# Kernel tuning notes

Hardware: AMD Instinct MI355X
Metric: run time of the kernel (lower is better)

Reference implementation:

```python
import jax, jax.numpy as jnp
import numpy as np


def setup_inputs() -> dict:
    key = jax.random.key(0)
    ks = jax.random.split(key, 7)
    B, N, Fin, Fout = 32, 1024, 64, 64
    s = 1.0 / np.sqrt(Fin)
    return {
        "X": jax.random.normal(ks[0], (B, N, Fin), dtype=jnp.float32),
        "A": jax.random.normal(ks[1], (B, N, N), dtype=jnp.float32),  # unused in forward, kept for signature fidelity
        "W": jax.random.uniform(ks[2], (Fin, Fout), jnp.float32, -s, s),
        "att_W": jax.random.uniform(ks[3], (Fin, Fout), jnp.float32, -s, s),
        "a": jax.random.uniform(ks[4], (Fout, Fout), jnp.float32, -s, s),
        "bias_W": jax.random.uniform(ks[5], (Fout,), jnp.float32, -s, s),
        "self_W": jax.random.uniform(ks[6], (Fin, Fout), jnp.float32, -s, s),
    }


def reference(X, A, W, att_W, a, bias_W, self_W):
    # att_X = X @ att_W : [B, N, Fout]
    att_X = jnp.einsum('bnf,fg->bng', X, att_W)
    # torch einsum 'ij,ajk->ajk' sums `a` over i => per-feature scale a.sum(0)
    scale = jnp.sum(a, axis=0)  # [Fout]
    # Z[b,i,k] = sum_j att_X[b,i,j] * scale[j] * att_X[b,k,j]  -> [B, N, N]
    Z = jnp.einsum('big,bkg->bik', att_X * scale, att_X)
    n = Z.shape[1]
    Z = Z * (1.0 - jnp.eye(n, dtype=Z.dtype))  # zero diagonal per batch
    att = jax.nn.leaky_relu(Z, negative_slope=0.01)
    # H = att @ (X W) + bias_W + X self_W
    XW = jnp.einsum('bnf,fg->bng', X, W)
    H = jnp.einsum('bnm,bmg->bng', att, XW) + bias_W
    H = H + jnp.einsum('bnf,fg->bng', X, self_W)
    return H
```

## Files before the change

### kernel.cpp

```cpp
#include <hip/hip_runtime.h>

#define DEV __device__ __forceinline__
typedef short s16x8 __attribute__((ext_vector_type(8)));
typedef float f32x16 __attribute__((ext_vector_type(16)));
typedef unsigned short u16;

#define WAIT_VMCNT(N) asm volatile("s_waitcnt vmcnt(" #N ")" ::: "memory")
#define CFENCE asm volatile("" ::: "memory")

DEV unsigned cvt_pk_bf16(float lo, float hi) {
  unsigned r;
  asm volatile("v_cvt_pk_bf16_f32 %0, %1, %2" : "=v"(r) : "v"(lo), "v"(hi));
  return r;
}
DEV u16 f2bf(float f) {
  unsigned u = __builtin_bit_cast(unsigned, f);
  unsigned r = u + 0x7fffu + ((u >> 16) & 1u);
  return (u16)(r >> 16);
}
DEV float bf2f(u16 u) { return __builtin_bit_cast(float, (unsigned)u << 16); }
DEV f32x16 zero16() {
  f32x16 v;
  #pragma unroll
  for (int i = 0; i < 16; ++i) v[i] = 0.f;
  return v;
}

DEV void gld16(const u16* g, u16* l) {
  __builtin_amdgcn_global_load_lds(
      (const __attribute__((address_space(1))) void*)g,
      (__attribute__((address_space(3))) void*)l, 16, 0, 0);
}

DEV void stage_tile64(const u16* __restrict__ gbase, size_t stride, u16* lbuf, int t) {
  #pragma unroll
  for (int p = 0; p < 2; ++p) {
    int c = p * 256 + t;
    int row = c >> 3, s = c & 7;
    int gck = s ^ (row & 7);
    const u16* src = gbase + (size_t)row * stride + gck * 8;
    u16* dst = lbuf + (size_t)(p * 256 + (t & 192)) * 8;
    gld16(src, dst);
  }
}

DEV s16x8 frag(const u16* buf, int row, int chunk) {
  return *(const s16x8*)(buf + row * 64 + ((chunk ^ (row & 7)) << 3));
}

DEV int kswz(int row, int d) {
  return row * 64 + ((((d >> 3) ^ (row & 7)) << 3) | (d & 7));
}

__global__ __launch_bounds__(256) void wprep_kernel(
    const float* __restrict__ attW, const float* __restrict__ W,
    const float* __restrict__ selfW, const float* __restrict__ Aa,
    u16* __restrict__ Wsw, float* __restrict__ scal_ws) {
  __shared__ __align__(16) u16 T[64 * 72];
  __shared__ float sc4[4][64];
  const int t = threadIdx.x, bi = blockIdx.x;

  if (bi == 0) {
    int qt = t >> 6, d = t & 63;
    float s = 0.f;
    #pragma unroll
    for (int i = 0; i < 16; ++i) s += Aa[(qt * 16 + i) * 64 + d];
    sc4[qt][d] = s;
  }

  const float* src = (bi == 0) ? attW : (bi == 1) ? W : selfW;
  #pragma unroll
  for (int p = 0; p < 4; ++p) {
    int c = p * 256 + t;
    int f = c >> 4, g0 = (c & 15) * 4;
    float4 v = *(const float4*)(src + f * 64 + g0);
    T[(g0 + 0) * 72 + f] = f2bf(v.x);
    T[(g0 + 1) * 72 + f] = f2bf(v.y);
    T[(g0 + 2) * 72 + f] = f2bf(v.z);
    T[(g0 + 3) * 72 + f] = f2bf(v.w);
  }
  __syncthreads();
  #pragma unroll
  for (int p = 0; p < 2; ++p) {
    int c = p * 256 + t;
    int g = c >> 3, f0 = (c & 7) * 8;
    *(s16x8*)&Wsw[bi * 4096 + g * 64 + f0] = *(const s16x8*)&T[g * 72 + f0];
  }
  if (bi == 0 && t < 64)
    scal_ws[t] = sc4[0][t] + sc4[1][t] + sc4[2][t] + sc4[3][t];
}

__global__ __launch_bounds__(256) void prep_kernel(
    const float* __restrict__ X, const u16* __restrict__ Wsw,
    const float* __restrict__ scal_ws, const float* __restrict__ biasW,
    u16* __restrict__ Kbf, u16* __restrict__ Qbf, u16* __restrict__ Vt,
    u16* __restrict__ Bb) {
  __shared__ __align__(16) u16 Xl[64 * 64];
  __shared__ __align__(16) u16 WtL[3][64 * 64];
  __shared__ __align__(16) u16 Ql[64 * 64];
  __shared__ __align__(16) u16 Bl[64 * 64];
  __shared__ __align__(16) u16 Vl[64 * 72];

  const int t = threadIdx.x;
  const int r0 = blockIdx.x * 64;
  const int b = r0 >> 10;
  const int n0 = r0 & 1023;
  const int lane = t & 63, w = t >> 6, h = lane >> 5, ln = lane & 31;
  const int rg = (w >> 1) * 32;
  const int cf = w & 1;
  const int d = cf * 32 + ln;

  #pragma unroll
  for (int i = 0; i < 3; ++i) stage_tile64(Wsw + i * 4096, 64, &WtL[i][0], t);

  const float sc_d = scal_ws[d];
  const float bi = biasW[d];

  #pragma unroll
  for (int p = 0; p < 2; ++p) {
    int c = p * 256 + t;
    int row = c >> 3, ck = c & 7;
    const float4* src = (const float4*)(X + (size_t)(r0 + row) * 64 + ck * 8);
    float4 a0 = src[0], a1 = src[1];
    unsigned* dst = (unsigned*)&Xl[row * 64 + ((ck ^ (row & 7)) << 3)];
    dst[0] = cvt_pk_bf16(a0.x, a0.y);
    dst[1] = cvt_pk_bf16(a0.z, a0.w);
    dst[2] = cvt_pk_bf16(a1.x, a1.y);
    dst[3] = cvt_pk_bf16(a1.z, a1.w);
  }
  __syncthreads();

  s16x8 xa[4];
  #pragma unroll
  for (int ks = 0; ks < 4; ++ks) xa[ks] = frag(Xl, rg + ln, ks * 2 + h);

  f32x16 aA = zero16(), aW = zero16(), aS = zero16();
  #pragma unroll
  for (int ks = 0; ks < 4; ++ks) {
    s16x8 bA = frag(&WtL[0][0], d, ks * 2 + h);
    s16x8 bW = frag(&WtL[1][0], d, ks * 2 + h);
    s16x8 bS = frag(&WtL[2][0], d, ks * 2 + h);
    aA = __builtin_amdgcn_mfma_f32_32x32x16_bf16(xa[ks], bA, aA, 0, 0, 0);
    aW = __builtin_amdgcn_mfma_f32_32x32x16_bf16(xa[ks], bW, aW, 0, 0, 0);
    aS = __builtin_amdgcn_mfma_f32_32x32x16_bf16(xa[ks], bS, aS, 0, 0, 0);
  }
  __syncthreads();

  #pragma unroll
  for (int reg = 0; reg < 16; ++reg) {
    int rl = (reg & 3) + 8 * (reg >> 2) + 4 * h;
    int row = rg + rl;
    Xl[kswz(row, d)] = f2bf(aA[reg]);
    Ql[kswz(row, d)] = f2bf(aA[reg] * sc_d);
    Bl[kswz(row, d)] = f2bf(aS[reg] + bi);
  }
  #pragma unroll
  for (int pg = 0; pg < 4; ++pg) {
    int n = rg + pg * 8 + 4 * h;
    *(unsigned*)&Vl[d * 72 + n] = cvt_pk_bf16(aW[pg * 4 + 0], aW[pg * 4 + 1]);
    *(unsigned*)&Vl[d * 72 + n + 2] = cvt_pk_bf16(aW[pg * 4 + 2], aW[pg * 4 + 3]);
  }
  __syncthreads();

  #pragma unroll
  for (int p = 0; p < 2; ++p) {
    int c = p * 256 + t;
    int row = c >> 3, ck = c & 7;
    size_t go = (size_t)(r0 + row) * 64 + ck * 8;
    int lo = row * 64 + ((ck ^ (row & 7)) << 3);
    *(s16x8*)&Kbf[go] = *(const s16x8*)&Xl[lo];
    *(s16x8*)&Qbf[go] = *(const s16x8*)&Ql[lo];
    *(s16x8*)&Bb[go] = *(const s16x8*)&Bl[lo];
  }
  #pragma unroll
  for (int p = 0; p < 2; ++p) {
    int c = p * 256 + t;
    int dd = c >> 3, ck = c & 7;
    *(s16x8*)&Vt[(size_t)(b * 64 + dd) * 1024 + n0 + ck * 8] =
        *(const s16x8*)&Vl[dd * 72 + ck * 8];
  }
}

#define PROC(SV, DG, PWV)                                                      \
  do {                                                                         \
    float p_[16];                                                              \
    _Pragma("unroll") for (int r_ = 0; r_ < 16; ++r_) {                        \
      float v_ = (SV)[r_];                                                     \
      p_[r_] = fmaxf(v_, 0.f) + 0.01f * fminf(v_, 0.f);                        \
    }                                                                          \
    if (DG) {                                                                  \
      _Pragma("unroll") for (int r_ = 0; r_ < 16; ++r_) {                      \
        int rl_ = (r_ & 3) + 8 * (r_ >> 2) + 4 * h;                            \
        p_[r_] = (rl_ == ln) ? 0.f : p_[r_];                                   \
      }                                                                        \
    }                                                                          \
    unsigned pk_[8];                                                           \
    _Pragma("unroll") for (int i_ = 0; i_ < 8; ++i_)                           \
        pk_[i_] = cvt_pk_bf16(p_[2 * i_], p_[2 * i_ + 1]);                     \
    auto a0_ = __builtin_amdgcn_permlane32_swap(pk_[0], pk_[2], false, false); \
    auto a1_ = __builtin_amdgcn_permlane32_swap(pk_[1], pk_[3], false, false); \
    auto a2_ = __builtin_amdgcn_permlane32_swap(pk_[4], pk_[6], false, false); \
    auto a3_ = __builtin_amdgcn_permlane32_swap(pk_[5], pk_[7], false, false); \
    PWV[0][0] = a0_[0]; PWV[0][1] = a1_[0]; PWV[0][2] = a0_[1];                \
    PWV[0][3] = a1_[1]; PWV[1][0] = a2_[0]; PWV[1][1] = a3_[0];                \
    PWV[1][2] = a2_[1]; PWV[1][3] = a3_[1];                                    \
  } while (0)

__global__ __launch_bounds__(256) void attn_kernel(
    const u16* __restrict__ Qbf, const u16* __restrict__ Kbf,
    const u16* __restrict__ Vt, const u16* __restrict__ Bb,
    float* __restrict__ Hout) {
  __shared__ __align__(16) u16 KV[3][2][64 * 64];
  float* Ol0 = (float*)&KV[0][0][0];
  float* Ol1 = (float*)&KV[1][0][0];

  const int t = threadIdx.x;
  const int b = blockIdx.x;
  const int q0 = blockIdx.y * 64;
  const int lane = t & 63, w = t >> 6, h = lane >> 5, ln = lane & 31;
  const int qh = w & 1, kvh = w >> 1;
  const int qg = q0 + qh * 32 + ln;

  const u16* Qg = Qbf + (size_t)b * 65536;
  const u16* Kg = Kbf + (size_t)b * 65536;
  const u16* Vg = Vt + (size_t)b * 65536;

  s16x8 qf[4];
  #pragma unroll
  for (int ks = 0; ks < 4; ++ks)
    qf[ks] = *(const s16x8*)(Qg + (size_t)qg * 64 + ks * 16 + h * 8);

  stage_tile64(Kg, 64, &KV[0][0][0], t);
  stage_tile64(Vg, 1024, &KV[0][1][0], t);
  stage_tile64(Kg + (size_t)64 * 64, 64, &KV[1][0][0], t);
  stage_tile64(Vg + 64, 1024, &KV[1][1][0], t);

  f32x16 o0 = zero16(), o1 = zero16();

  #pragma unroll 1
  for (int tix = 0; tix < 16; ++tix) {
    const int kv0 = tix * 64;
    if (tix < 15) {
      WAIT_VMCNT(4);
    } else {
      WAIT_VMCNT(0);
    }
    __builtin_amdgcn_s_barrier();
    CFENCE;
    if (tix < 14) {
      const int ns = (tix + 2) % 3;
      stage_tile64(Kg + (size_t)(kv0 + 128) * 64, 64, &KV[ns][0][0], t);
      stage_tile64(Vg + (kv0 + 128), 1024, &KV[ns][1][0], t);
    }
    const u16* Kl = &KV[tix % 3][0][0];
    const u16* Vl = &KV[tix % 3][1][0];

    f32x16 s = zero16();
    __builtin_amdgcn_s_setprio(1);
    #pragma unroll
    for (int ks = 0; ks < 4; ++ks)
      s = __builtin_amdgcn_mfma_f32_32x32x16_bf16(frag(Kl, kvh * 32 + ln, ks * 2 + h), qf[ks], s, 0, 0, 0);
    __builtin_amdgcn_s_setprio(0);

    const bool dg = (kv0 + kvh * 32) == (q0 + qh * 32);
    unsigned pw[2][4];
    PROC(s, dg, pw);

    __builtin_amdgcn_s_setprio(1);
    #pragma unroll
    for (int kk = 0; kk < 2; ++kk) {
      union { unsigned u[4]; s16x8 v; } pb;
      pb.u[0] = pw[kk][0]; pb.u[1] = pw[kk][1];
      pb.u[2] = pw[kk][2]; pb.u[3] = pw[kk][3];
      int ch = kvh * 4 + kk * 2 + h;
      o0 = __builtin_amdgcn_mfma_f32_32x32x16_bf16(frag(Vl, ln, ch), pb.v, o0, 0, 0, 0);
      o1 = __builtin_amdgcn_mfma_f32_32x32x16_bf16(frag(Vl, 32 + ln, ch), pb.v, o1, 0, 0, 0);
    }
    __builtin_amdgcn_s_setprio(0);
  }

  __syncthreads();

  float* Od = kvh ? Ol1 : Ol0;
  const int q = qh * 32 + ln;
  #pragma unroll
  for (int reg = 0; reg < 16; ++reg) {
    int rl = (reg & 3) + 8 * (reg >> 2) + 4 * h;
    int d0 = rl, d1 = 32 + rl;
    Od[q * 64 + ((((d0 >> 2) ^ (q & 15)) << 2) | (d0 & 3))] = o0[reg];
    Od[q * 64 + ((((d1 >> 2) ^ (q & 15)) << 2) | (d1 & 3))] = o1[reg];
  }
  __syncthreads();
  #pragma unroll
  for (int i = 0; i < 4; ++i) {
    int fi = i * 256 + t;
    int qq = fi >> 4, g = fi & 15;
    int off = qq * 64 + ((g ^ (qq & 15)) << 2);
    float4 v0 = *(const float4*)&Ol0[off];
    float4 v1 = *(const float4*)&Ol1[off];
    size_t go = ((size_t)b * 1024 + q0 + qq) * 64 + g * 4;
    const short4 bv = *(const short4*)(Bb + go);
    float4 v;
    v.x = v0.x + v1.x + bf2f((u16)bv.x);
    v.y = v0.y + v1.y + bf2f((u16)bv.y);
    v.z = v0.z + v1.z + bf2f((u16)bv.z);
    v.w = v0.w + v1.w + bf2f((u16)bv.w);
    *(float4*)(Hout + go) = v;
  }
}

extern "C" void kernel_launch(void* const* d_in, const int* in_sizes, int n_in,
                              void* d_out, int out_size, void* d_ws, size_t ws_size,
                              hipStream_t stream) {
  const float* X = (const float*)d_in[0];
  const float* W = (const float*)d_in[2];
  const float* attW = (const float*)d_in[3];
  const float* a = (const float*)d_in[4];
  const float* biasW = (const float*)d_in[5];
  const float* selfW = (const float*)d_in[6];
  float* H = (float*)d_out;

  u16* Kbf = (u16*)d_ws;
  u16* Qbf = Kbf + (size_t)32 * 1024 * 64;
  u16* Vt = Qbf + (size_t)32 * 1024 * 64;
  u16* Bb = Vt + (size_t)32 * 1024 * 64;
  u16* Wsw = Bb + (size_t)32 * 1024 * 64;
  float* scal = (float*)(Wsw + 3 * 4096);

  wprep_kernel<<<3, 256, 0, stream>>>(attW, W, selfW, a, Wsw, scal);
  prep_kernel<<<512, 256, 0, stream>>>(X, Wsw, scal, biasW, Kbf, Qbf, Vt, Bb);
  attn_kernel<<<dim3(32, 16), 256, 0, stream>>>(Qbf, Kbf, Vt, Bb, H);
}
```

Measured before the change: 37.72 us.

## Load K/V MFMA fragments directly from global into registers, drop LDS staging

The attention kernel no longer stages K and V tiles through a triple-buffered LDS ring guarded by barriers. Each wave now loads its own MFMA operand fragments straight from global memory into registers, prefetching the next tile one iteration ahead. This removes per-tile barriers and LDS traffic but issues smaller, less coalesced global loads, and the V loads stride across rows. The prep kernel grid is also changed to 2D indexing, which is equivalent to the old 1D mapping.

```diff
diff --git a/kernel.cpp b/kernel.cpp
--- a/kernel.cpp
+++ b/kernel.cpp
@@ -4,9 +4,6 @@
 typedef short s16x8 __attribute__((ext_vector_type(8)));
 typedef float f32x16 __attribute__((ext_vector_type(16)));
 typedef unsigned short u16;
-
-#define WAIT_VMCNT(N) asm volatile("s_waitcnt vmcnt(" #N ")" ::: "memory")
-#define CFENCE asm volatile("" ::: "memory")
 
 DEV unsigned cvt_pk_bf16(float lo, float hi) {
   unsigned r;
@@ -102,9 +99,9 @@
   __shared__ __align__(16) u16 Vl[64 * 72];
 
   const int t = threadIdx.x;
-  const int r0 = blockIdx.x * 64;
-  const int b = r0 >> 10;
-  const int n0 = r0 & 1023;
+  const int b = blockIdx.x;
+  const int n0 = blockIdx.y * 64;
+  const int r0 = b * 1024 + n0;
   const int lane = t & 63, w = t >> 6, h = lane >> 5, ln = lane & 31;
   const int rg = (w >> 1) * 32;
   const int cf = w & 1;
@@ -210,9 +207,8 @@
     const u16* __restrict__ Qbf, const u16* __restrict__ Kbf,
     const u16* __restrict__ Vt, const u16* __restrict__ Bb,
     float* __restrict__ Hout) {
-  __shared__ __align__(16) u16 KV[3][2][64 * 64];
-  float* Ol0 = (float*)&KV[0][0][0];
-  float* Ol1 = (float*)&KV[1][0][0];
+  __shared__ __align__(16) float Ol0[64 * 64];
+  __shared__ __align__(16) float Ol1[64 * 64];
 
   const int t = threadIdx.x;
   const int b = blockIdx.x;
@@ -230,56 +226,58 @@
   for (int ks = 0; ks < 4; ++ks)
     qf[ks] = *(const s16x8*)(Qg + (size_t)qg * 64 + ks * 16 + h * 8);
 
-  stage_tile64(Kg, 64, &KV[0][0][0], t);
-  stage_tile64(Vg, 1024, &KV[0][1][0], t);
-  stage_tile64(Kg + (size_t)64 * 64, 64, &KV[1][0][0], t);
-  stage_tile64(Vg + 64, 1024, &KV[1][1][0], t);
-
   f32x16 o0 = zero16(), o1 = zero16();
 
-  #pragma unroll 1
+  s16x8 kfc[4], vfc[4];
+  #pragma unroll
+  for (int ks = 0; ks < 4; ++ks)
+    kfc[ks] = *(const s16x8*)(Kg + (size_t)(kvh * 32 + ln) * 64 + ks * 16 + h * 8);
+  #pragma unroll
+  for (int kk = 0; kk < 2; ++kk) {
+    int co = kvh * 32 + kk * 16 + h * 8;
+    vfc[kk * 2] = *(const s16x8*)(Vg + (size_t)ln * 1024 + co);
+    vfc[kk * 2 + 1] = *(const s16x8*)(Vg + (size_t)(32 + ln) * 1024 + co);
+  }
+
+  #pragma unroll 2
   for (int tix = 0; tix < 16; ++tix) {
     const int kv0 = tix * 64;
+
+    s16x8 kfn[4], vfn[4];
     if (tix < 15) {
-      WAIT_VMCNT(4);
-    } else {
-      WAIT_VMCNT(0);
+      const int nb = kv0 + 64 + kvh * 32;
+      #pragma unroll
+      for (int ks = 0; ks < 4; ++ks)
+        kfn[ks] = *(const s16x8*)(Kg + (size_t)(nb + ln) * 64 + ks * 16 + h * 8);
+      #pragma unroll
+      for (int kk = 0; kk < 2; ++kk) {
+        int co = nb + kk * 16 + h * 8;
+        vfn[kk * 2] = *(const s16x8*)(Vg + (size_t)ln * 1024 + co);
+        vfn[kk * 2 + 1] = *(const s16x8*)(Vg + (size_t)(32 + ln) * 1024 + co);
+      }
     }
-    __builtin_amdgcn_s_barrier();
-    CFENCE;
-    if (tix < 14) {
-      const int ns = (tix + 2) % 3;
-      stage_tile64(Kg + (size_t)(kv0 + 128) * 64, 64, &KV[ns][0][0], t);
-      stage_tile64(Vg + (kv0 + 128), 1024, &KV[ns][1][0], t);
-    }
-    const u16* Kl = &KV[tix % 3][0][0];
-    const u16* Vl = &KV[tix % 3][1][0];
 
     f32x16 s = zero16();
-    __builtin_amdgcn_s_setprio(1);
     #pragma unroll
     for (int ks = 0; ks < 4; ++ks)
-      s = __builtin_amdgcn_mfma_f32_32x32x16_bf16(frag(Kl, kvh * 32 + ln, ks * 2 + h), qf[ks], s, 0, 0, 0);
-    __builtin_amdgcn_s_setprio(0);
+      s = __builtin_amdgcn_mfma_f32_32x32x16_bf16(kfc[ks], qf[ks], s, 0, 0, 0);
 
     const bool dg = (kv0 + kvh * 32) == (q0 + qh * 32);
     unsigned pw[2][4];
     PROC(s, dg, pw);
 
-    __builtin_amdgcn_s_setprio(1);
     #pragma unroll
     for (int kk = 0; kk < 2; ++kk) {
       union { unsigned u[4]; s16x8 v; } pb;
       pb.u[0] = pw[kk][0]; pb.u[1] = pw[kk][1];
       pb.u[2] = pw[kk][2]; pb.u[3] = pw[kk][3];
-      int ch = kvh * 4 + kk * 2 + h;
-      o0 = __builtin_amdgcn_mfma_f32_32x32x16_bf16(frag(Vl, ln, ch), pb.v, o0, 0, 0, 0);
-      o1 = __builtin_amdgcn_mfma_f32_32x32x16_bf16(frag(Vl, 32 + ln, ch), pb.v, o1, 0, 0, 0);
+      o0 = __builtin_amdgcn_mfma_f32_32x32x16_bf16(vfc[kk * 2], pb.v, o0, 0, 0, 0);
+      o1 = __builtin_amdgcn_mfma_f32_32x32x16_bf16(vfc[kk * 2 + 1], pb.v, o1, 0, 0, 0);
     }
-    __builtin_amdgcn_s_setprio(0);
-  }
-
-  __syncthreads();
+
+    #pragma unroll
+    for (int i = 0; i < 4; ++i) { kfc[i] = kfn[i]; vfc[i] = vfn[i]; }
+  }
 
   float* Od = kvh ? Ol1 : Ol0;
   const int q = qh * 32 + ln;
@@ -328,6 +326,6 @@
   float* scal = (float*)(Wsw + 3 * 4096);
 
   wprep_kernel<<<3, 256, 0, stream>>>(attW, W, selfW, a, Wsw, scal);
-  prep_kernel<<<512, 256, 0, stream>>>(X, Wsw, scal, biasW, Kbf, Qbf, Vt, Bb);
+  prep_kernel<<<dim3(32, 16), 256, 0, stream>>>(X, Wsw, scal, biasW, Kbf, Qbf, Vt, Bb);
   attn_kernel<<<dim3(32, 16), 256, 0, stream>>>(Qbf, Kbf, Vt, Bb, H);
 }
```

After: 48.40 us. 28.3% more time.
